# Performance work log

Measured on AMD Instinct MI355X. Metric: run time of the kernel, lower is better.

## Reference

```python
import jax, jax.numpy as jnp
import numpy as np

B, N, C = 8, 1024, 768
H = 12
D = C // H  # head_dim = 64
SCALE = D ** -0.5
EPS = 1e-5


def _layer_norm(x):
    # per-head LayerNorm over last dim, gamma=1, beta=0, biased variance
    mean = x.mean(-1, keepdims=True)
    var = ((x - mean) ** 2).mean(-1, keepdims=True)
    return (x - mean) / jnp.sqrt(var + EPS)


def setup_inputs() -> dict:
    key = jax.random.key(0)
    k1, k2, k3 = jax.random.split(key, 3)
    x = jax.random.normal(k1, (B, N, C), dtype=jnp.float32)
    qkv_weight = jax.random.normal(k2, (3 * C, C), dtype=jnp.float32) * (C ** -0.5)
    proj_weight = jax.random.normal(k3, (C, C), dtype=jnp.float32) * (C ** -0.5)
    return {"x": x, "qkv_weight": qkv_weight, "proj_weight": proj_weight}


def reference(x, qkv_weight, proj_weight):
    Bx, Nx, Cx = x.shape
    qkv = x @ qkv_weight.T                          # [B,N,3C]
    qkv = qkv.reshape(Bx, Nx, 3, H, D).transpose(2, 0, 3, 1, 4)  # [3,B,H,N,D]
    q, k, v = qkv[0], qkv[1], qkv[2]
    q = _layer_norm(q) * SCALE
    k = _layer_norm(k)
    attn = jnp.einsum('bhnd,bhmd->bhnm', q, k)      # [B,H,N,N]
    attn = jax.nn.softmax(attn, axis=-1)
    out = jnp.einsum('bhnm,bhmd->bhnd', attn, v)    # [B,H,N,D]
    out = out.transpose(0, 2, 1, 3).reshape(Bx, Nx, Cx)
    return out @ proj_weight.T
```

## Files before the change

kernel.cpp:

```cpp
#include <hip/hip_runtime.h>
#include <stdint.h>
#include <stddef.h>

#define HB 8
#define HN 1024
#define HC 768
#define HH 12
#define HD 64
#define ROWS (HB*HN)
#define BH (HB*HH)

using s16x4  = __attribute__((ext_vector_type(4))) short;
using bf16x8 = __attribute__((ext_vector_type(8))) short;
using f32x4  = __attribute__((ext_vector_type(4))) float;

__device__ __forceinline__ short f2bf(float f) {
  union { float f; uint32_t u; } c; c.f = f;
  uint32_t u = c.u;
  uint32_t r = (u + 0x7fffu + ((u >> 16) & 1u)) >> 16;
  return (short)r;
}
__device__ __forceinline__ float bf2f(short s) {
  union { uint32_t u; float f; } c; c.u = ((uint32_t)(uint16_t)s) << 16;
  return c.f;
}
__device__ __forceinline__ uint32_t pack_bf16_rne(float a, float b) {
  union { float f; uint32_t u; } ca, cb; ca.f = a; cb.f = b;
  uint32_t ra = ca.u + 0x7fffu + ((ca.u >> 16) & 1u);
  uint32_t rb = cb.u + 0x7fffu + ((cb.u >> 16) & 1u);
  return __builtin_amdgcn_perm(rb, ra, 0x07060302);
}
__device__ __forceinline__ float fast_exp2(float x) {
#if __has_builtin(__builtin_amdgcn_exp2f)
  return __builtin_amdgcn_exp2f(x);
#else
  return exp2f(x);
#endif
}
__device__ __forceinline__ f32x4 mfma16(bf16x8 a, bf16x8 b, f32x4 c) {
  return __builtin_amdgcn_mfma_f32_16x16x32_bf16(a, b, c, 0, 0, 0);
}
__device__ __forceinline__ void gll16(const void* g, void* l) {
  __builtin_amdgcn_global_load_lds((const __attribute__((address_space(1))) void*)g,
                                   (__attribute__((address_space(3))) void*)l,
                                   16, 0, 0);
}

__global__ void cvt3_kernel(const float* __restrict__ x,  short* __restrict__ xb,  int n0,
                            const float* __restrict__ wq, short* __restrict__ wqb, int n1,
                            const float* __restrict__ wp, short* __restrict__ wpb, int n2) {
  int i = blockIdx.x * 256 + threadIdx.x;
  const float* in; short* out;
  if (i < n0)            { in = x;  out = xb;  }
  else if (i < n0 + n1)  { i -= n0; in = wq; out = wqb; }
  else if (i < n0 + n1 + n2) { i -= n0 + n1; in = wp; out = wpb; }
  else return;
  float4 v = ((const float4*)in)[i];
  s16x4 o;
  o.x = f2bf(v.x); o.y = f2bf(v.y); o.z = f2bf(v.z); o.w = f2bf(v.w);
  ((s16x4*)out)[i] = o;
}

__device__ __forceinline__ void store_c(float* p, float v) { *p = v; }
__device__ __forceinline__ void store_c(short* p, float v) { *p = f2bf(v); }

__global__ __launch_bounds__(256) void gemm_qkv(const short* __restrict__ A,
                                                const short* __restrict__ Bw,
                                                short* __restrict__ Qb,
                                                short* __restrict__ Kb,
                                                short* __restrict__ vb) {
  const int K = HC;
  __shared__ short As[128*64];
  __shared__ short Bs[128*64];
  const int m0 = blockIdx.y * 128, n0 = blockIdx.x * 128;
  const int tid = threadIdx.x;
  const int lane = tid & 63, w = tid >> 6, quad = lane >> 4, lc = lane & 15;
  const int wr = w >> 1, wc = w & 1;
  f32x4 acc[4][4] = {};
  for (int kt = 0; kt < K; kt += 64) {
#pragma unroll
    for (int i = 0; i < 4; ++i) {
      const int chunk = i*256 + tid;
      const int r = chunk >> 3, cb = chunk & 7;
      const int cbs = cb ^ (r & 7);
      gll16(A  + (size_t)(m0 + r)*K + kt + cbs*8, (void*)(As + (size_t)chunk*8));
      gll16(Bw + (size_t)(n0 + r)*K + kt + cbs*8, (void*)(Bs + (size_t)chunk*8));
    }
    __syncthreads();
#pragma unroll
    for (int kk = 0; kk < 2; ++kk) {
      bf16x8 af[4], bfr[4];
      const int kb = kk*4 + quad;
#pragma unroll
      for (int mt = 0; mt < 4; ++mt)
        af[mt] = *(const bf16x8*)(As + (wr*64 + mt*16 + lc)*64 + (kb ^ (lc & 7))*8);
#pragma unroll
      for (int nt = 0; nt < 4; ++nt)
        bfr[nt] = *(const bf16x8*)(Bs + (wc*64 + nt*16 + lc)*64 + (kb ^ (lc & 7))*8);
#pragma unroll
      for (int mt = 0; mt < 4; ++mt)
#pragma unroll
        for (int nt = 0; nt < 4; ++nt)
          acc[mt][nt] = mfma16(af[mt], bfr[nt], acc[mt][nt]);
    }
    __syncthreads();
  }
  const int cg = n0 + wc*64;
  const int t = cg / HC;
  const int h = (cg % HC) / HD;
  const int b = m0 >> 10;
  const int bh = b*HH + h;
  if (t < 2) {
    short* outp = (t == 0) ? Qb : Kb;
    const float sc = (t == 0) ? 0.125f : 1.0f;
#pragma unroll
    for (int mt = 0; mt < 4; ++mt)
#pragma unroll
      for (int r = 0; r < 4; ++r) {
        float s1 = (acc[mt][0][r] + acc[mt][1][r]) + (acc[mt][2][r] + acc[mt][3][r]);
        float s2 = acc[mt][0][r]*acc[mt][0][r];
        s2 = __builtin_fmaf(acc[mt][1][r], acc[mt][1][r], s2);
        s2 = __builtin_fmaf(acc[mt][2][r], acc[mt][2][r], s2);
        s2 = __builtin_fmaf(acc[mt][3][r], acc[mt][3][r], s2);
#pragma unroll
        for (int off = 1; off < 16; off <<= 1) {
          s1 += __shfl_xor(s1, off);
          s2 += __shfl_xor(s2, off);
        }
        const float mean = s1 * (1.0f/64.0f);
        const float var  = s2 * (1.0f/64.0f) - mean*mean;
        const float inv  = rsqrtf(var + 1e-5f) * sc;
        const int n_in = (m0 & 1023) + wr*64 + mt*16 + quad*4 + r;
        short* rowp = outp + ((size_t)bh*HN + n_in)*HD;
#pragma unroll
        for (int nt = 0; nt < 4; ++nt)
          rowp[nt*16 + lc] = f2bf((acc[mt][nt][r] - mean) * inv);
      }
  } else {
#pragma unroll
    for (int mt = 0; mt < 4; ++mt)
#pragma unroll
      for (int nt = 0; nt < 4; ++nt)
#pragma unroll
        for (int r = 0; r < 4; ++r) {
          const int row = m0 + wr*64 + mt*16 + quad*4 + r;
          const int col = h*HD + nt*16 + lc;
          vb[(size_t)row*HC + col] = f2bf(acc[mt][nt][r]);
        }
  }
}

__global__ __launch_bounds__(256) void gemm_bt_f32(const short* __restrict__ A,
                                                   const short* __restrict__ Bw,
                                                   float* __restrict__ C,
                                                   int M, int N, int K) {
  __shared__ short As[128*64];
  __shared__ short Bs[128*64];
  const int m0 = blockIdx.y * 128, n0 = blockIdx.x * 128;
  const int tid = threadIdx.x;
  const int lane = tid & 63, w = tid >> 6, quad = lane >> 4, lc = lane & 15;
  const int wr = w >> 1, wc = w & 1;
  f32x4 acc[4][4] = {};
  for (int kt = 0; kt < K; kt += 64) {
#pragma unroll
    for (int i = 0; i < 4; ++i) {
      const int chunk = i*256 + tid;
      const int r = chunk >> 3, cb = chunk & 7;
      const int cbs = cb ^ (r & 7);
      gll16(A  + (size_t)(m0 + r)*K + kt + cbs*8, (void*)(As + (size_t)chunk*8));
      gll16(Bw + (size_t)(n0 + r)*K + kt + cbs*8, (void*)(Bs + (size_t)chunk*8));
    }
    __syncthreads();
#pragma unroll
    for (int kk = 0; kk < 2; ++kk) {
      bf16x8 af[4], bfr[4];
      const int kb = kk*4 + quad;
#pragma unroll
      for (int mt = 0; mt < 4; ++mt)
        af[mt] = *(const bf16x8*)(As + (wr*64 + mt*16 + lc)*64 + (kb ^ (lc & 7))*8);
#pragma unroll
      for (int nt = 0; nt < 4; ++nt)
        bfr[nt] = *(const bf16x8*)(Bs + (wc*64 + nt*16 + lc)*64 + (kb ^ (lc & 7))*8);
#pragma unroll
      for (int mt = 0; mt < 4; ++mt)
#pragma unroll
        for (int nt = 0; nt < 4; ++nt)
          acc[mt][nt] = mfma16(af[mt], bfr[nt], acc[mt][nt]);
    }
    __syncthreads();
  }
#pragma unroll
  for (int mt = 0; mt < 4; ++mt)
#pragma unroll
    for (int nt = 0; nt < 4; ++nt)
#pragma unroll
      for (int r = 0; r < 4; ++r) {
        const int row = m0 + wr*64 + mt*16 + quad*4 + r;
        const int col = n0 + wc*64 + nt*16 + lc;
        store_c(C + (size_t)row*N + col, acc[mt][nt][r]);
      }
}

__global__ __launch_bounds__(256) void vtrans_kernel(const short* __restrict__ vb,
                                                     short* __restrict__ Vtb) {
  const int blk = blockIdx.x;
  const int tile = blk & 7, bh = blk >> 3;
  const int b = bh / HH, h = bh % HH;
  const int n0 = tile * 128;
  const int tid = threadIdx.x;
  __shared__ float vt[128][65];
#pragma unroll
  for (int i = 0; i < 32; ++i) {
    const int idx = i*256 + tid; const int r = idx >> 6, dcol = idx & 63;
    vt[r][dcol] = bf2f(vb[(size_t)(b*HN + n0 + r)*HC + h*HD + dcol]);
  }
  __syncthreads();
#pragma unroll
  for (int it = 0; it < 4; ++it) {
    const int idx = it*256 + tid;
    const int dd = idx >> 4, j8 = idx & 15;
    bf16x8 o;
#pragma unroll
    for (int u = 0; u < 8; ++u) {
      const int c  = j8*8 + u;
      const int g  = c >> 6, cl = c & 63;
      const int k  = g*64 + ((cl & 3)*16 + (cl >> 2));
      o[u] = f2bf(vt[k][dd]);
    }
    *(bf16x8*)(Vtb + ((size_t)bh*HD + dd)*HN + n0 + j8*8) = o;
  }
}

__global__ __launch_bounds__(256, 3) void attn_kernel(const short* __restrict__ Qb,
                                                      const short* __restrict__ Kb,
                                                      const short* __restrict__ Vtb,
                                                      short* __restrict__ AOb) {
  const int blk = blockIdx.x;
  const int qt = blk & 7, bh = blk >> 3;
  const int b = bh / HH, h = bh % HH;
  const int tid = threadIdx.x, w = tid >> 6, lane = tid & 63;
  const int quad = lane >> 4, lc = lane & 15;

  __shared__ short Ks [64][72];
  __shared__ short Vts[64][72];
  __shared__ short Ps [4][32][72];

  bf16x8 aq[2][2];
#pragma unroll
  for (int mt = 0; mt < 2; ++mt) {
    const int mrow = qt*128 + w*32 + mt*16 + lc;
    aq[mt][0] = *(const bf16x8*)(Qb + ((size_t)bh*HN + mrow)*HD + quad*8);
    aq[mt][1] = *(const bf16x8*)(Qb + ((size_t)bh*HN + mrow)*HD + 32 + quad*8);
  }

  const short* kbh = Kb  + (size_t)bh*HN*HD;
  const short* vbh = Vtb + (size_t)bh*HD*HN;

  f32x4 oacc[2][4] = {};
  float l_i[2][4] = {};

  bf16x8 gk[2], gv[2];
#pragma unroll
  for (int i = 0; i < 2; ++i) {
    const int c = i*256 + tid;
    gk[i] = *(const bf16x8*)(kbh + (size_t)(c >> 3)*HD + (c & 7)*8);
    gv[i] = *(const bf16x8*)(vbh + (size_t)(c >> 3)*HN + (c & 7)*8);
  }
#pragma unroll
  for (int i = 0; i < 2; ++i) {
    const int c = i*256 + tid;
    *(bf16x8*)(&Ks [c >> 3][(c & 7)*8]) = gk[i];
    *(bf16x8*)(&Vts[c >> 3][(c & 7)*8]) = gv[i];
  }
  __syncthreads();

  const float LOG2E = 1.44269504f;
  const float MB2   = 8.0f * 1.44269504f;

  for (int ck = 0; ck < 16; ++ck) {
    if (ck < 15) {
      const int nn0 = (ck + 1)*64;
#pragma unroll
      for (int i = 0; i < 2; ++i) {
        const int c = i*256 + tid;
        gk[i] = *(const bf16x8*)(kbh + (size_t)(nn0 + (c >> 3))*HD + (c & 7)*8);
        gv[i] = *(const bf16x8*)(vbh + (size_t)(c >> 3)*HN + nn0 + (c & 7)*8);
      }
    }

    f32x4 sacc[2][4] = {};
#pragma unroll
    for (int kk = 0; kk < 2; ++kk)
#pragma unroll
      for (int nt = 0; nt < 4; ++nt) {
        bf16x8 bk = *(const bf16x8*)(&Ks[nt*16 + lc][kk*32 + quad*8]);
#pragma unroll
        for (int mt = 0; mt < 2; ++mt)
          sacc[mt][nt] = mfma16(aq[mt][kk], bk, sacc[mt][nt]);
      }

#pragma unroll
    for (int mt = 0; mt < 2; ++mt)
#pragma unroll
      for (int r = 0; r < 4; ++r) {
        float ps[4];
#pragma unroll
        for (int nt = 0; nt < 4; ++nt) {
          ps[nt] = fast_exp2(__builtin_fmaf(sacc[mt][nt][r], LOG2E, -MB2));
          sacc[mt][nt][r] = ps[nt];
        }
        l_i[mt][r] += (ps[0] + ps[1]) + (ps[2] + ps[3]);
        uint2 pk;
        pk.x = pack_bf16_rne(ps[0], ps[1]);
        pk.y = pack_bf16_rne(ps[2], ps[3]);
        *(uint2*)(&Ps[w][mt*16 + quad*4 + r][lc*4]) = pk;
      }

#pragma unroll
    for (int kk = 0; kk < 2; ++kk) {
      bf16x8 ap[2];
#pragma unroll
      for (int mt = 0; mt < 2; ++mt)
        ap[mt] = *(const bf16x8*)(&Ps[w][mt*16 + lc][kk*32 + quad*8]);
#pragma unroll
      for (int nt2 = 0; nt2 < 4; ++nt2) {
        bf16x8 bv = *(const bf16x8*)(&Vts[nt2*16 + lc][kk*32 + quad*8]);
#pragma unroll
        for (int mt = 0; mt < 2; ++mt)
          oacc[mt][nt2] = mfma16(ap[mt], bv, oacc[mt][nt2]);
      }
    }

    if (ck < 15) {
      __syncthreads();
#pragma unroll
      for (int i = 0; i < 2; ++i) {
        const int c = i*256 + tid;
        *(bf16x8*)(&Ks [c >> 3][(c & 7)*8]) = gk[i];
        *(bf16x8*)(&Vts[c >> 3][(c & 7)*8]) = gv[i];
      }
      __syncthreads();
    }
  }

#pragma unroll
  for (int mt = 0; mt < 2; ++mt)
#pragma unroll
    for (int r = 0; r < 4; ++r) {
      float l = l_i[mt][r];
#pragma unroll
      for (int off = 1; off < 16; off <<= 1) l += __shfl_xor(l, off);
      const float rl = 1.0f / l;
      const int row = qt*128 + w*32 + mt*16 + quad*4 + r;
#pragma unroll
      for (int nt2 = 0; nt2 < 4; ++nt2) {
        const int d = nt2*16 + lc;
        AOb[((size_t)(b*HN + row))*HC + h*HD + d] = f2bf(oacc[mt][nt2][r] * rl);
      }
    }
}

extern "C" void kernel_launch(void* const* d_in, const int* in_sizes, int n_in,
                              void* d_out, int out_size, void* d_ws, size_t ws_size,
                              hipStream_t stream) {
  const float* x     = (const float*)d_in[0];
  const float* wqkv  = (const float*)d_in[1];
  const float* wproj = (const float*)d_in[2];
  float* out = (float*)d_out;

  char* ws = (char*)d_ws;
  size_t off = 0;
  auto alloc = [&](size_t bytes) -> void* {
    void* p = ws + off; off += (bytes + 255) & ~(size_t)255; return p;
  };
  short* xb     = (short*)alloc((size_t)ROWS*HC*2);
  short* wqkvb  = (short*)alloc((size_t)3*HC*HC*2);
  short* wprojb = (short*)alloc((size_t)HC*HC*2);
  short* vb     = (short*)alloc((size_t)ROWS*HC*2);
  short* Qb     = (short*)alloc((size_t)BH*HN*HD*2);
  short* Kb     = (short*)alloc((size_t)BH*HN*HD*2);
  short* Vtb    = (short*)alloc((size_t)BH*HD*HN*2);
  short* AOb    = (short*)alloc((size_t)ROWS*HC*2);

  { const int n0 = ROWS*HC/4, n1 = 3*HC*HC/4, n2 = HC*HC/4;
    const int tot = n0 + n1 + n2;
    cvt3_kernel<<<(tot + 255)/256, 256, 0, stream>>>(x, xb, n0, wqkv, wqkvb, n1,
                                                     wproj, wprojb, n2); }

  gemm_qkv<<<dim3(3*HC/128, ROWS/128), 256, 0, stream>>>(xb, wqkvb, Qb, Kb, vb);
  vtrans_kernel<<<BH*8, 256, 0, stream>>>(vb, Vtb);
  attn_kernel<<<BH*8, 256, 0, stream>>>(Qb, Kb, Vtb, AOb);
  gemm_bt_f32<<<dim3(HC/128, ROWS/128), 256, 0, stream>>>(AOb, wprojb, out,
                                                          ROWS, HC, HC);
}
```

Before: 204.0 us.

## Rewrite QKV GEMM with 256x256 tiles and a 4-stage async LDS pipeline

The QKV projection GEMM moves from 128x128 tiles with synchronous per-k loads to 256x256 tiles using 512 threads. Operands are streamed through a 4-deep LDS ring with a K-step of 32, so global loads for later stages overlap with MFMA work on the current stage. Waits on outstanding loads use explicit vmcnt counts, and MFMA sections are bracketed by barriers and s_setprio. Blocks are launched on a 1D grid with a swizzle intended to improve L2 reuse. The larger tile raises register pressure (a 32-entry accumulator array) and leaves only 288 workgroups to spread across the GPU.

New measurement: 204.6 us. Within noise of the previous version (+0.3%).

```diff
diff --git a/kernel.cpp b/kernel.cpp
--- a/kernel.cpp
+++ b/kernel.cpp
@@ -64,64 +64,126 @@
 __device__ __forceinline__ void store_c(float* p, float v) { *p = v; }
 __device__ __forceinline__ void store_c(short* p, float v) { *p = f2bf(v); }
 
-__global__ __launch_bounds__(256) void gemm_qkv(const short* __restrict__ A,
-                                                const short* __restrict__ Bw,
-                                                short* __restrict__ Qb,
-                                                short* __restrict__ Kb,
-                                                short* __restrict__ vb) {
-  const int K = HC;
-  __shared__ short As[128*64];
-  __shared__ short Bs[128*64];
-  const int m0 = blockIdx.y * 128, n0 = blockIdx.x * 128;
+template<int VM, bool STG>
+__device__ __forceinline__ void qkv_ktstep(
+    int kt, short* sA, short* sB,
+    const short* Ag, const short* Bg,
+    int wr, int wc, int quad, int lc,
+    int c0, int c1, int r0, int r1, int sc0, int sc1,
+    f32x4 (&acc)[8][4])
+{
+  const short* sa = sA + (kt & 3) * 8192;
+  const short* sb = sB + (kt & 3) * 8192;
+  short* dA = sA + ((kt + 3) & 3) * 8192;
+  short* dB = sB + ((kt + 3) & 3) * 8192;
+  const int kcol = (kt + 3) * 32;
+
+  bf16x8 bfr[4], af[4];
+#pragma unroll
+  for (int nt = 0; nt < 4; ++nt) {
+    const int rB = wc*64 + nt*16 + lc;
+    bfr[nt] = *(const bf16x8*)(sb + rB*32 + (quad ^ ((rB >> 1) & 3))*8);
+  }
+#pragma unroll
+  for (int mt = 0; mt < 4; ++mt) {
+    const int rA = wr*128 + mt*16 + lc;
+    af[mt] = *(const bf16x8*)(sa + rA*32 + (quad ^ ((rA >> 1) & 3))*8);
+  }
+  if constexpr (STG) {
+    gll16(Ag + (size_t)r0*HC + kcol + sc0, (void*)(dA + c0*8));
+    gll16(Ag + (size_t)r1*HC + kcol + sc1, (void*)(dA + c1*8));
+  }
+  asm volatile("s_barrier" ::: "memory");
+  __builtin_amdgcn_s_setprio(1);
+#pragma unroll
+  for (int mt = 0; mt < 4; ++mt)
+#pragma unroll
+    for (int nt = 0; nt < 4; ++nt)
+      acc[mt][nt] = mfma16(af[mt], bfr[nt], acc[mt][nt]);
+  __builtin_amdgcn_s_setprio(0);
+  asm volatile("s_barrier" ::: "memory");
+#pragma unroll
+  for (int mt = 0; mt < 4; ++mt) {
+    const int rA = wr*128 + 64 + mt*16 + lc;
+    af[mt] = *(const bf16x8*)(sa + rA*32 + (quad ^ ((rA >> 1) & 3))*8);
+  }
+  if constexpr (STG) {
+    gll16(Bg + (size_t)r0*HC + kcol + sc0, (void*)(dB + c0*8));
+    gll16(Bg + (size_t)r1*HC + kcol + sc1, (void*)(dB + c1*8));
+  }
+  asm volatile("s_barrier" ::: "memory");
+  __builtin_amdgcn_s_setprio(1);
+#pragma unroll
+  for (int mt = 0; mt < 4; ++mt)
+#pragma unroll
+    for (int nt = 0; nt < 4; ++nt)
+      acc[4+mt][nt] = mfma16(af[mt], bfr[nt], acc[4+mt][nt]);
+  __builtin_amdgcn_s_setprio(0);
+  if constexpr (VM == 8)      asm volatile("s_waitcnt vmcnt(8)" ::: "memory");
+  else if constexpr (VM == 4) asm volatile("s_waitcnt vmcnt(4)" ::: "memory");
+  else if constexpr (VM == 0) asm volatile("s_waitcnt vmcnt(0)" ::: "memory");
+  asm volatile("s_barrier" ::: "memory");
+}
+
+__global__ __launch_bounds__(512, 2) void gemm_qkv(const short* __restrict__ A,
+                                                   const short* __restrict__ Bw,
+                                                   short* __restrict__ Qb,
+                                                   short* __restrict__ Kb,
+                                                   short* __restrict__ vb) {
+  __shared__ short As[4*256*32];
+  __shared__ short Bs[4*256*32];
+  const int wg = blockIdx.x;
+  const int swz = (wg & 7)*36 + (wg >> 3);
+  const int bx = swz % 9, by = swz / 9;
+  const int m0 = by*256, n0 = bx*256;
   const int tid = threadIdx.x;
   const int lane = tid & 63, w = tid >> 6, quad = lane >> 4, lc = lane & 15;
-  const int wr = w >> 1, wc = w & 1;
-  f32x4 acc[4][4] = {};
-  for (int kt = 0; kt < K; kt += 64) {
-#pragma unroll
-    for (int i = 0; i < 4; ++i) {
-      const int chunk = i*256 + tid;
-      const int r = chunk >> 3, cb = chunk & 7;
-      const int cbs = cb ^ (r & 7);
-      gll16(A  + (size_t)(m0 + r)*K + kt + cbs*8, (void*)(As + (size_t)chunk*8));
-      gll16(Bw + (size_t)(n0 + r)*K + kt + cbs*8, (void*)(Bs + (size_t)chunk*8));
-    }
-    __syncthreads();
-#pragma unroll
-    for (int kk = 0; kk < 2; ++kk) {
-      bf16x8 af[4], bfr[4];
-      const int kb = kk*4 + quad;
-#pragma unroll
-      for (int mt = 0; mt < 4; ++mt)
-        af[mt] = *(const bf16x8*)(As + (wr*64 + mt*16 + lc)*64 + (kb ^ (lc & 7))*8);
-#pragma unroll
-      for (int nt = 0; nt < 4; ++nt)
-        bfr[nt] = *(const bf16x8*)(Bs + (wc*64 + nt*16 + lc)*64 + (kb ^ (lc & 7))*8);
-#pragma unroll
-      for (int mt = 0; mt < 4; ++mt)
-#pragma unroll
-        for (int nt = 0; nt < 4; ++nt)
-          acc[mt][nt] = mfma16(af[mt], bfr[nt], acc[mt][nt]);
-    }
-    __syncthreads();
-  }
+  const int wr = w >> 2, wc = w & 3;
+  const int c0 = tid, c1 = 512 + tid;
+  const int r0 = c0 >> 2, cb0 = c0 & 3;
+  const int r1 = c1 >> 2, cb1 = c1 & 3;
+  const int sc0 = (cb0 ^ ((r0 >> 1) & 3))*8;
+  const int sc1 = (cb1 ^ ((r1 >> 1) & 3))*8;
+  const short* Ag = A  + (size_t)m0*HC;
+  const short* Bg = Bw + (size_t)n0*HC;
+  f32x4 acc[8][4] = {};
+
+#pragma unroll
+  for (int pk = 0; pk < 3; ++pk) {
+    gll16(Ag + (size_t)r0*HC + pk*32 + sc0, (void*)(As + pk*8192 + c0*8));
+    gll16(Ag + (size_t)r1*HC + pk*32 + sc1, (void*)(As + pk*8192 + c1*8));
+    gll16(Bg + (size_t)r0*HC + pk*32 + sc0, (void*)(Bs + pk*8192 + c0*8));
+    gll16(Bg + (size_t)r1*HC + pk*32 + sc1, (void*)(Bs + pk*8192 + c1*8));
+  }
+  asm volatile("s_waitcnt vmcnt(8)" ::: "memory");
+  asm volatile("s_barrier" ::: "memory");
+
+#pragma unroll 1
+  for (int kt = 0; kt < 21; ++kt)
+    qkv_ktstep<8,true >(kt, As, Bs, Ag, Bg, wr, wc, quad, lc,
+                        c0, c1, r0, r1, sc0, sc1, acc);
+  qkv_ktstep<4,false>(21, As, Bs, Ag, Bg, wr, wc, quad, lc,
+                      c0, c1, r0, r1, sc0, sc1, acc);
+  qkv_ktstep<0,false>(22, As, Bs, Ag, Bg, wr, wc, quad, lc,
+                      c0, c1, r0, r1, sc0, sc1, acc);
+  qkv_ktstep<-1,false>(23, As, Bs, Ag, Bg, wr, wc, quad, lc,
+                       c0, c1, r0, r1, sc0, sc1, acc);
+
   const int cg = n0 + wc*64;
   const int t = cg / HC;
   const int h = (cg % HC) / HD;
-  const int b = m0 >> 10;
-  const int bh = b*HH + h;
   if (t < 2) {
     short* outp = (t == 0) ? Qb : Kb;
     const float sc = (t == 0) ? 0.125f : 1.0f;
 #pragma unroll
-    for (int mt = 0; mt < 4; ++mt)
+    for (int i = 0; i < 8; ++i)
 #pragma unroll
       for (int r = 0; r < 4; ++r) {
-        float s1 = (acc[mt][0][r] + acc[mt][1][r]) + (acc[mt][2][r] + acc[mt][3][r]);
-        float s2 = acc[mt][0][r]*acc[mt][0][r];
-        s2 = __builtin_fmaf(acc[mt][1][r], acc[mt][1][r], s2);
-        s2 = __builtin_fmaf(acc[mt][2][r], acc[mt][2][r], s2);
-        s2 = __builtin_fmaf(acc[mt][3][r], acc[mt][3][r], s2);
+        float s1 = (acc[i][0][r] + acc[i][1][r]) + (acc[i][2][r] + acc[i][3][r]);
+        float s2 = acc[i][0][r]*acc[i][0][r];
+        s2 = __builtin_fmaf(acc[i][1][r], acc[i][1][r], s2);
+        s2 = __builtin_fmaf(acc[i][2][r], acc[i][2][r], s2);
+        s2 = __builtin_fmaf(acc[i][3][r], acc[i][3][r], s2);
 #pragma unroll
         for (int off = 1; off < 16; off <<= 1) {
           s1 += __shfl_xor(s1, off);
@@ -130,22 +192,23 @@
         const float mean = s1 * (1.0f/64.0f);
         const float var  = s2 * (1.0f/64.0f) - mean*mean;
         const float inv  = rsqrtf(var + 1e-5f) * sc;
-        const int n_in = (m0 & 1023) + wr*64 + mt*16 + quad*4 + r;
-        short* rowp = outp + ((size_t)bh*HN + n_in)*HD;
+        const int row = m0 + wr*128 + i*16 + quad*4 + r;
+        const int b = row >> 10, n_in = row & 1023;
+        short* rowp = outp + ((size_t)(b*HH + h)*HN + n_in)*HD;
 #pragma unroll
         for (int nt = 0; nt < 4; ++nt)
-          rowp[nt*16 + lc] = f2bf((acc[mt][nt][r] - mean) * inv);
+          rowp[nt*16 + lc] = f2bf((acc[i][nt][r] - mean) * inv);
       }
   } else {
 #pragma unroll
-    for (int mt = 0; mt < 4; ++mt)
+    for (int i = 0; i < 8; ++i)
 #pragma unroll
       for (int nt = 0; nt < 4; ++nt)
 #pragma unroll
         for (int r = 0; r < 4; ++r) {
-          const int row = m0 + wr*64 + mt*16 + quad*4 + r;
+          const int row = m0 + wr*128 + i*16 + quad*4 + r;
           const int col = h*HD + nt*16 + lc;
-          vb[(size_t)row*HC + col] = f2bf(acc[mt][nt][r]);
+          vb[(size_t)row*HC + col] = f2bf(acc[i][nt][r]);
         }
   }
 }
@@ -387,7 +450,7 @@
     cvt3_kernel<<<(tot + 255)/256, 256, 0, stream>>>(x, xb, n0, wqkv, wqkvb, n1,
                                                      wproj, wprojb, n2); }
 
-  gemm_qkv<<<dim3(3*HC/128, ROWS/128), 256, 0, stream>>>(xb, wqkvb, Qb, Kb, vb);
+  gemm_qkv<<<dim3(288), 512, 0, stream>>>(xb, wqkvb, Qb, Kb, vb);
   vtrans_kernel<<<BH*8, 256, 0, stream>>>(vb, Vtb);
   attn_kernel<<<BH*8, 256, 0, stream>>>(Qb, Kb, Vtb, AOb);
   gemm_bt_f32<<<dim3(HC/128, ROWS/128), 256, 0, stream>>>(AOb, wprojb, out,
```

## Restructure QKV GEMM with triple-buffered async loads and larger tiles

Applied to the files above, without the earlier changes.

Rewrites the QKV projection GEMM to use 256x128 tiles with 512 threads (8 waves), a 3-stage LDS ring buffer with K-step 32, and vmcnt-based waits so global loads for tile k+2 overlap MFMA work on tile k. It also adds a grouped block-index swizzle for L2 locality and raises wave priority around the MFMA block. The aim is to hide global-load latency and cut per-iteration double barriers. The cost is more LDS per block and more complex hand-scheduled synchronization that relies on exact vmcnt counts.

After: 200.4 us. Within noise of the previous version (-1.8%).

```diff
diff --git a/kernel.cpp b/kernel.cpp
--- a/kernel.cpp
+++ b/kernel.cpp
@@ -64,64 +64,111 @@
 __device__ __forceinline__ void store_c(float* p, float v) { *p = v; }
 __device__ __forceinline__ void store_c(short* p, float v) { *p = f2bf(v); }
 
-__global__ __launch_bounds__(256) void gemm_qkv(const short* __restrict__ A,
-                                                const short* __restrict__ Bw,
-                                                short* __restrict__ Qb,
-                                                short* __restrict__ Kb,
-                                                short* __restrict__ vb) {
-  const int K = HC;
-  __shared__ short As[128*64];
-  __shared__ short Bs[128*64];
-  const int m0 = blockIdx.y * 128, n0 = blockIdx.x * 128;
+template<int VM, bool STG, int SLOT>
+__device__ __forceinline__ void qkv_ktile(
+    int kt, short* sA, short* sB,
+    const short* Ag, const short* Bg,
+    int wr, int wc, int quad, int lc,
+    int aoff0, int aoff1, int boff0,
+    int cA0, int cA1, int cB0,
+    f32x4 (&acc)[4][4])
+{
+  if constexpr (VM == 3) asm volatile("s_waitcnt vmcnt(3)" ::: "memory");
+  else                   asm volatile("s_waitcnt vmcnt(0)" ::: "memory");
+  __builtin_amdgcn_s_barrier();
+  if constexpr (STG) {
+    constexpr int DST = (SLOT + 2) % 3;
+    const int kcol = (kt + 2) * 32;
+    short* dA = sA + DST*8192;
+    short* dB = sB + DST*4096;
+    gll16(Ag + (size_t)(aoff0 + kcol), (void*)(dA + cA0*8));
+    gll16(Ag + (size_t)(aoff1 + kcol), (void*)(dA + cA1*8));
+    gll16(Bg + (size_t)(boff0 + kcol), (void*)(dB + cB0*8));
+  }
+  const short* sa = sA + SLOT*8192;
+  const short* sb = sB + SLOT*4096;
+  bf16x8 af[4], bfr[4];
+#pragma unroll
+  for (int mt = 0; mt < 4; ++mt) {
+    const int rA = wr*64 + mt*16 + lc;
+    af[mt] = *(const bf16x8*)(sa + rA*32 + (quad ^ ((rA >> 1) & 3))*8);
+  }
+#pragma unroll
+  for (int nt = 0; nt < 4; ++nt) {
+    const int rB = wc*64 + nt*16 + lc;
+    bfr[nt] = *(const bf16x8*)(sb + rB*32 + (quad ^ ((rB >> 1) & 3))*8);
+  }
+  __builtin_amdgcn_s_setprio(1);
+#pragma unroll
+  for (int mt = 0; mt < 4; ++mt)
+#pragma unroll
+    for (int nt = 0; nt < 4; ++nt)
+      acc[mt][nt] = mfma16(af[mt], bfr[nt], acc[mt][nt]);
+  __builtin_amdgcn_s_setprio(0);
+}
+
+__global__ __launch_bounds__(512, 4) void gemm_qkv(const short* __restrict__ A,
+                                                   const short* __restrict__ Bw,
+                                                   short* __restrict__ Qb,
+                                                   short* __restrict__ Kb,
+                                                   short* __restrict__ vb) {
+  __shared__ short As[3*256*32];
+  __shared__ short Bs[3*128*32];
+  const int wg = blockIdx.x;
+  const int swz = (wg & 7)*72 + (wg >> 3);
+  const int by = swz / 18, bx = swz % 18;
+  const int m0 = by*256, n0 = bx*128;
   const int tid = threadIdx.x;
   const int lane = tid & 63, w = tid >> 6, quad = lane >> 4, lc = lane & 15;
   const int wr = w >> 1, wc = w & 1;
+  const int cA0 = tid,        rA0 = cA0 >> 2, sbA0 = ((cA0 & 3) ^ ((rA0 >> 1) & 3))*8;
+  const int cA1 = 512 + tid,  rA1 = cA1 >> 2, sbA1 = ((cA1 & 3) ^ ((rA1 >> 1) & 3))*8;
+  const int cB0 = tid,        rB0 = cB0 >> 2, sbB0 = ((cB0 & 3) ^ ((rB0 >> 1) & 3))*8;
+  const int aoff0 = rA0*HC + sbA0;
+  const int aoff1 = rA1*HC + sbA1;
+  const int boff0 = rB0*HC + sbB0;
+  const short* Ag = A  + (size_t)m0*HC;
+  const short* Bg = Bw + (size_t)n0*HC;
   f32x4 acc[4][4] = {};
-  for (int kt = 0; kt < K; kt += 64) {
-#pragma unroll
-    for (int i = 0; i < 4; ++i) {
-      const int chunk = i*256 + tid;
-      const int r = chunk >> 3, cb = chunk & 7;
-      const int cbs = cb ^ (r & 7);
-      gll16(A  + (size_t)(m0 + r)*K + kt + cbs*8, (void*)(As + (size_t)chunk*8));
-      gll16(Bw + (size_t)(n0 + r)*K + kt + cbs*8, (void*)(Bs + (size_t)chunk*8));
-    }
-    __syncthreads();
-#pragma unroll
-    for (int kk = 0; kk < 2; ++kk) {
-      bf16x8 af[4], bfr[4];
-      const int kb = kk*4 + quad;
-#pragma unroll
-      for (int mt = 0; mt < 4; ++mt)
-        af[mt] = *(const bf16x8*)(As + (wr*64 + mt*16 + lc)*64 + (kb ^ (lc & 7))*8);
-#pragma unroll
-      for (int nt = 0; nt < 4; ++nt)
-        bfr[nt] = *(const bf16x8*)(Bs + (wc*64 + nt*16 + lc)*64 + (kb ^ (lc & 7))*8);
-#pragma unroll
-      for (int mt = 0; mt < 4; ++mt)
-#pragma unroll
-        for (int nt = 0; nt < 4; ++nt)
-          acc[mt][nt] = mfma16(af[mt], bfr[nt], acc[mt][nt]);
-    }
-    __syncthreads();
-  }
+
+#pragma unroll
+  for (int pk = 0; pk < 2; ++pk) {
+    gll16(Ag + (size_t)(aoff0 + pk*32), (void*)(As + pk*8192 + cA0*8));
+    gll16(Ag + (size_t)(aoff1 + pk*32), (void*)(As + pk*8192 + cA1*8));
+    gll16(Bg + (size_t)(boff0 + pk*32), (void*)(Bs + pk*4096 + cB0*8));
+  }
+
+#pragma unroll 1
+  for (int kt = 0; kt < 21; kt += 3) {
+    qkv_ktile<3,true,0>(kt,   As, Bs, Ag, Bg, wr, wc, quad, lc,
+                        aoff0, aoff1, boff0, cA0, cA1, cB0, acc);
+    qkv_ktile<3,true,1>(kt+1, As, Bs, Ag, Bg, wr, wc, quad, lc,
+                        aoff0, aoff1, boff0, cA0, cA1, cB0, acc);
+    qkv_ktile<3,true,2>(kt+2, As, Bs, Ag, Bg, wr, wc, quad, lc,
+                        aoff0, aoff1, boff0, cA0, cA1, cB0, acc);
+  }
+  qkv_ktile<3,true ,0>(21, As, Bs, Ag, Bg, wr, wc, quad, lc,
+                       aoff0, aoff1, boff0, cA0, cA1, cB0, acc);
+  qkv_ktile<3,false,1>(22, As, Bs, Ag, Bg, wr, wc, quad, lc,
+                       aoff0, aoff1, boff0, cA0, cA1, cB0, acc);
+  qkv_ktile<0,false,2>(23, As, Bs, Ag, Bg, wr, wc, quad, lc,
+                       aoff0, aoff1, boff0, cA0, cA1, cB0, acc);
+
   const int cg = n0 + wc*64;
   const int t = cg / HC;
   const int h = (cg % HC) / HD;
-  const int b = m0 >> 10;
-  const int bh = b*HH + h;
   if (t < 2) {
     short* outp = (t == 0) ? Qb : Kb;
     const float sc = (t == 0) ? 0.125f : 1.0f;
 #pragma unroll
-    for (int mt = 0; mt < 4; ++mt)
+    for (int i = 0; i < 4; ++i)
 #pragma unroll
       for (int r = 0; r < 4; ++r) {
-        float s1 = (acc[mt][0][r] + acc[mt][1][r]) + (acc[mt][2][r] + acc[mt][3][r]);
-        float s2 = acc[mt][0][r]*acc[mt][0][r];
-        s2 = __builtin_fmaf(acc[mt][1][r], acc[mt][1][r], s2);
-        s2 = __builtin_fmaf(acc[mt][2][r], acc[mt][2][r], s2);
-        s2 = __builtin_fmaf(acc[mt][3][r], acc[mt][3][r], s2);
+        float s1 = (acc[i][0][r] + acc[i][1][r]) + (acc[i][2][r] + acc[i][3][r]);
+        float s2 = acc[i][0][r]*acc[i][0][r];
+        s2 = __builtin_fmaf(acc[i][1][r], acc[i][1][r], s2);
+        s2 = __builtin_fmaf(acc[i][2][r], acc[i][2][r], s2);
+        s2 = __builtin_fmaf(acc[i][3][r], acc[i][3][r], s2);
 #pragma unroll
         for (int off = 1; off < 16; off <<= 1) {
           s1 += __shfl_xor(s1, off);
@@ -130,22 +177,23 @@
         const float mean = s1 * (1.0f/64.0f);
         const float var  = s2 * (1.0f/64.0f) - mean*mean;
         const float inv  = rsqrtf(var + 1e-5f) * sc;
-        const int n_in = (m0 & 1023) + wr*64 + mt*16 + quad*4 + r;
-        short* rowp = outp + ((size_t)bh*HN + n_in)*HD;
+        const int row = m0 + wr*64 + i*16 + quad*4 + r;
+        const int b = row >> 10, n_in = row & 1023;
+        short* rowp = outp + ((size_t)(b*HH + h)*HN + n_in)*HD;
 #pragma unroll
         for (int nt = 0; nt < 4; ++nt)
-          rowp[nt*16 + lc] = f2bf((acc[mt][nt][r] - mean) * inv);
+          rowp[nt*16 + lc] = f2bf((acc[i][nt][r] - mean) * inv);
       }
   } else {
 #pragma unroll
-    for (int mt = 0; mt < 4; ++mt)
+    for (int i = 0; i < 4; ++i)
 #pragma unroll
       for (int nt = 0; nt < 4; ++nt)
 #pragma unroll
         for (int r = 0; r < 4; ++r) {
-          const int row = m0 + wr*64 + mt*16 + quad*4 + r;
+          const int row = m0 + wr*64 + i*16 + quad*4 + r;
           const int col = h*HD + nt*16 + lc;
-          vb[(size_t)row*HC + col] = f2bf(acc[mt][nt][r]);
+          vb[(size_t)row*HC + col] = f2bf(acc[i][nt][r]);
         }
   }
 }
@@ -387,7 +435,7 @@
     cvt3_kernel<<<(tot + 255)/256, 256, 0, stream>>>(x, xb, n0, wqkv, wqkvb, n1,
                                                      wproj, wprojb, n2); }
 
-  gemm_qkv<<<dim3(3*HC/128, ROWS/128), 256, 0, stream>>>(xb, wqkvb, Qb, Kb, vb);
+  gemm_qkv<<<dim3(576), 512, 0, stream>>>(xb, wqkvb, Qb, Kb, vb);
   vtrans_kernel<<<BH*8, 256, 0, stream>>>(vb, Vtb);
   attn_kernel<<<BH*8, 256, 0, stream>>>(Qb, Kb, Vtb, AOb);
   gemm_bt_f32<<<dim3(HC/128, ROWS/128), 256, 0, stream>>>(AOb, wprojb, out,
```
